# Kernel optimization log

Measured on AMD Instinct MI355X. Metric: run time of the kernel, lower is better.

## Reference

```python
import jax, jax.numpy as jnp
import numpy as np

K = 3  # Chebyshev filter size (max_view)


def avwgcn(X, E, weights_pool, bias_pool):
    """Adaptive node-wise graph conv. X: [B,N,C_in], E: [N,D]."""
    N = E.shape[0]
    # adaptive adjacency: softmax over rows of relu(E E^T)
    supports = jax.nn.softmax(jax.nn.relu(E @ E.T), axis=1)  # [N,N]
    support_set = [jnp.eye(N, dtype=X.dtype), supports]
    for _ in range(2, K):  # Chebyshev recursion
        support_set.append(2.0 * supports @ support_set[-1] - support_set[-2])
    S = jnp.stack(support_set, axis=0)  # [K,N,N]
    W = jnp.einsum('nd,dkio->nkio', E, weights_pool)  # per-node weights [N,K,Ci,Co]
    bias = E @ bias_pool  # [N,Co]
    XG = jnp.einsum('knm,bmc->bnkc', S, X)  # [B,N,K,Ci]
    return jnp.einsum('bnki,nkio->bno', XG, W) + bias  # [B,N,Co]


def setup_inputs() -> dict:
    key = jax.random.key(0)
    ks = jax.random.split(key, 5)
    B, N, Cin, Cout, D = 32, 4096, 2, 64, 10
    Ci = Cin + Cout  # 66
    X = jax.random.normal(ks[0], (B, N, Cin), dtype=jnp.float32)
    H = jnp.zeros((B, N, Cout), dtype=jnp.float32)
    E = jax.random.normal(ks[1], (N, D), dtype=jnp.float32)
    W_gate = jax.random.normal(ks[2], (D, K, Ci, 2 * Cout), dtype=jnp.float32) * 0.1
    b_gate = jnp.zeros((D, 2 * Cout), dtype=jnp.float32)
    W_update = jax.random.normal(ks[3], (D, K, Ci, Cout), dtype=jnp.float32) * 0.1
    b_update = jnp.zeros((D, Cout), dtype=jnp.float32)
    return {"X": X, "H": H, "E": E, "W_gate": W_gate, "b_gate": b_gate,
            "W_update": W_update, "b_update": b_update}


def reference(X, H, E, W_gate, b_gate, W_update, b_update):
    Cout = H.shape[-1]
    XH = jnp.concatenate([X, H], axis=-1)  # [B,N,Cin+Cout]
    ZR = jax.nn.sigmoid(avwgcn(XH, E, W_gate, b_gate))  # [B,N,2*Cout]
    Z, R = ZR[..., :Cout], ZR[..., Cout:]
    C = jnp.concatenate([X, Z * H], axis=-1)
    HC = jnp.tanh(avwgcn(C, E, W_update, b_update))
    return R * H + (1.0 - R) * HC
```

## Files before the change

### kernel.cpp

```cpp
#include <hip/hip_runtime.h>
#include <math.h>

#define N_NODES 4096
#define BATCH   32
#define D_EMB   10
#define CIN     2
#define COUT    64
#define CI      66
#define KSUP    3
#define NCOLS   2112
#define NPAD    2176
#define LDT     4096

#define KI_REAL 198
#define KILD    232
#define OCH     (32 * KILD)
#define WROW_G  (128 * KILD)
#define WROW_U  (64 * KILD)
#define WGT2_R  (WROW_G + WROW_U)

typedef _Float16 half_t;
typedef __attribute__((ext_vector_type(8))) _Float16 f16x8;
typedef __attribute__((ext_vector_type(4))) _Float16 f16x4;
typedef __attribute__((ext_vector_type(2))) _Float16 f16x2;
typedef __attribute__((ext_vector_type(4))) float f32x4;

union u32h2 { unsigned u; f16x2 h; };

__device__ __forceinline__ float fast_sigmoid(float x) { return 1.f / (1.f + __expf(-x)); }
__device__ __forceinline__ float fast_tanh(float x) { return 1.f - 2.f / (__expf(2.f * x) + 1.f); }

__device__ __forceinline__ void gld_lds16(const half_t* g, half_t* l) {
  __builtin_amdgcn_global_load_lds(
      (const __attribute__((address_space(1))) void*)g,
      (__attribute__((address_space(3))) void*)l, 16, 0, 0);
}

__global__ __launch_bounds__(256) void k_softmax_p(const float* __restrict__ E,
                                                   half_t* __restrict__ Pb) {
  const int n = blockIdx.x;
  const int tid = threadIdx.x;
  __shared__ float En[D_EMB];
  __shared__ float ms[256], ss[256];
  if (tid < D_EMB) En[tid] = E[n * D_EMB + tid];
  __syncthreads();
  float en[D_EMB];
#pragma unroll
  for (int d = 0; d < D_EMB; ++d) en[d] = En[d];

  float m = -1e30f, s = 0.f;
  for (int c = tid; c < N_NODES; c += 256) {
    const float* Ec = E + c * D_EMB;
    float v = 0.f;
#pragma unroll
    for (int d = 0; d < D_EMB; ++d) v += en[d] * Ec[d];
    v = fmaxf(v, 0.f);
    if (v > m) { s *= __expf(m - v); m = v; }
    s += __expf(v - m);
  }
  ms[tid] = m; ss[tid] = s;
  __syncthreads();
  for (int off = 128; off > 0; off >>= 1) {
    if (tid < off) {
      float m2 = ms[tid + off], s2 = ss[tid + off];
      float m1 = ms[tid], s1 = ss[tid];
      float mm = fmaxf(m1, m2);
      ms[tid] = mm;
      ss[tid] = s1 * __expf(m1 - mm) + s2 * __expf(m2 - mm);
    }
    __syncthreads();
  }
  const float M = ms[0];
  const float inv = 1.f / ss[0];
  half_t* Pr = Pb + (size_t)n * N_NODES;
  for (int c = tid; c < N_NODES; c += 256) {
    const float* Ec = E + c * D_EMB;
    float v = 0.f;
#pragma unroll
    for (int d = 0; d < D_EMB; ++d) v += en[d] * Ec[d];
    v = fmaxf(v, 0.f);
    Pr[c] = (half_t)(__expf(v - M) * inv);
  }
}

__global__ __launch_bounds__(256) void k_build_v0(const float* __restrict__ X,
                                                  const float* __restrict__ H,
                                                  half_t* __restrict__ Vt,
                                                  half_t* __restrict__ Vn,
                                                  half_t* __restrict__ Cbt,
                                                  half_t* __restrict__ Cbn) {
  size_t idx = (size_t)blockIdx.x * 256 + threadIdx.x;
  if (idx >= (size_t)N_NODES * NCOLS) return;
  const int m = (int)(idx / NCOLS);
  const int col = (int)(idx % NCOLS);
  const int b = col / CI;
  const int c = col % CI;
  float v;
  if (c < CIN) v = X[((size_t)b * N_NODES + m) * CIN + c];
  else         v = H[((size_t)b * N_NODES + m) * COUT + (c - CIN)];
  const half_t h = (half_t)v;
  Vn[(size_t)m * NPAD + col] = h;
  Vt[(size_t)col * LDT + m] = h;
  if (c < CIN) {
    Cbn[(size_t)m * NPAD + col] = h;
    Cbt[(size_t)col * LDT + m] = h;
  }
}

__global__ __launch_bounds__(256) void k_gemm_f16(const half_t* __restrict__ A,
                                                  const half_t* __restrict__ Bt,
                                                  half_t* __restrict__ Cn,
                                                  half_t* __restrict__ Ct) {
  __shared__ half_t As[128 * 32];
  __shared__ half_t Bs[128 * 32];
  const int tid = threadIdx.x;
  const int lane = tid & 63;
  const int wave = tid >> 6;
  const int wm = (wave >> 1) * 64;
  const int wn = (wave & 1) * 64;
  const int rb = blockIdx.y * 128;
  const int cb = blockIdx.x * 128;

  const int srow = lane >> 2;
  const int skg = (((lane & 3) + ((lane >> 3) & 3)) & 3) * 8;
  const half_t* ga0 = A + (size_t)(rb + wave * 32 + srow) * N_NODES + skg;
  const half_t* ga1 = ga0 + (size_t)16 * N_NODES;
  const half_t* gb0 = Bt + (size_t)(cb + wave * 32 + srow) * LDT + skg;
  const half_t* gb1 = gb0 + (size_t)16 * LDT;
  half_t* lA0 = As + wave * 1024;
  half_t* lA1 = lA0 + 512;
  half_t* lB0 = Bs + wave * 1024;
  half_t* lB1 = lB0 + 512;

  const int fr = lane & 15;
  const int fg = lane >> 4;
  const int fofs = (4 * fr + ((fg - (fr >> 1)) & 3)) * 8;

  f32x4 acc[4][4] = {};

  for (int k0 = 0; k0 < N_NODES; k0 += 32) {
    __syncthreads();
    gld_lds16(ga0 + k0, lA0);
    gld_lds16(ga1 + k0, lA1);
    gld_lds16(gb0 + k0, lB0);
    gld_lds16(gb1 + k0, lB1);
    __syncthreads();

    f16x8 a[4], b[4];
#pragma unroll
    for (int i = 0; i < 4; ++i)
      a[i] = *(const f16x8*)&As[((wm >> 4) + i) * 512 + fofs];
#pragma unroll
    for (int j = 0; j < 4; ++j)
      b[j] = *(const f16x8*)&Bs[((wn >> 4) + j) * 512 + fofs];
#pragma unroll
    for (int i = 0; i < 4; ++i)
#pragma unroll
      for (int j = 0; j < 4; ++j)
        acc[i][j] = __builtin_amdgcn_mfma_f32_16x16x32_f16(a[i], b[j], acc[i][j], 0, 0, 0);
  }

  const int en = lane & 15;
  const int em = (lane >> 4) * 4;
#pragma unroll
  for (int i = 0; i < 4; ++i) {
#pragma unroll
    for (int j = 0; j < 4; ++j) {
      const int m0 = rb + wm + i * 16 + em;
      const int n = cb + wn + j * 16 + en;
      half_t h0 = (half_t)acc[i][j][0];
      half_t h1 = (half_t)acc[i][j][1];
      half_t h2 = (half_t)acc[i][j][2];
      half_t h3 = (half_t)acc[i][j][3];
      if (Ct) {
        f16x4 t4 = {h0, h1, h2, h3};
        *(f16x4*)&Ct[(size_t)n * LDT + m0] = t4;
      }
      Cn[(size_t)(m0 + 0) * NPAD + n] = h0;
      Cn[(size_t)(m0 + 1) * NPAD + n] = h1;
      Cn[(size_t)(m0 + 2) * NPAD + n] = h2;
      Cn[(size_t)(m0 + 3) * NPAD + n] = h3;
    }
  }
}

__global__ __launch_bounds__(256) void k_wgt2(const float* __restrict__ Wg,
                                              const float* __restrict__ Wu,
                                              unsigned* __restrict__ WT2) {
  const int r = blockIdx.x * 256 + threadIdx.x;
  if (r >= WGT2_R) return;
  const float* pool;
  int o, ki, ostr;
  if (r < WROW_G) { o = r / KILD; ki = r % KILD; pool = Wg; ostr = 128; }
  else { int r2 = r - WROW_G; o = r2 / KILD; ki = r2 % KILD; pool = Wu; ostr = 64; }
#pragma unroll
  for (int dp = 0; dp < 5; ++dp) {
    u32h2 v; v.h = f16x2{(half_t)0.f, (half_t)0.f};
    if (ki < KI_REAL) {
      const int k = ki / CI;
      const int i = ki % CI;
      v.h[0] = (half_t)pool[(((size_t)(2 * dp) * KSUP + k) * CI + i) * ostr + o];
      v.h[1] = (half_t)pool[(((size_t)(2 * dp + 1) * KSUP + k) * CI + i) * ostr + o];
    }
    WT2[(size_t)dp * WGT2_R + r] = v.u;
  }
}

__device__ __forceinline__ void stage_xg(const half_t* __restrict__ v0r,
                                         const half_t* __restrict__ g1r,
                                         const half_t* __restrict__ g2r,
                                         half_t* __restrict__ xg, int tid) {
  for (int idx = tid; idx < NCOLS / 8; idx += 256) {
    const f16x8 v0 = *(const f16x8*)&v0r[idx * 8];
    const f16x8 g1 = *(const f16x8*)&g1r[idx * 8];
    const f16x8 g2 = *(const f16x8*)&g2r[idx * 8];
    const f16x8 x2 = g2 + g2 - v0;
#pragma unroll
    for (int e = 0; e < 8; ++e) {
      const int col = idx * 8 + e;
      const int b = col / CI;
      const int i = col - b * CI;
      xg[b * KILD + i] = v0[e];
      xg[b * KILD + CI + i] = g1[e];
      xg[b * KILD + 2 * CI + i] = x2[e];
    }
  }
  for (int z = tid; z < 32 * 17; z += 256) {
    const int b = z / 17;
    const int j = z - b * 17;
    *(unsigned*)&xg[b * KILD + KI_REAL + j * 2] = 0u;
  }
}

__global__ __launch_bounds__(256) void k_gate_t(const half_t* __restrict__ Vn,
                                                const half_t* __restrict__ G1n,
                                                const half_t* __restrict__ G2n,
                                                const unsigned* __restrict__ WT2,
                                                const float* __restrict__ E,
                                                const float* __restrict__ bg,
                                                const float* __restrict__ H,
                                                half_t* __restrict__ Cbn,
                                                half_t* __restrict__ Cbt,
                                                half_t* __restrict__ Rb) {
  const int n0 = blockIdx.x * 2;
  const int tid = threadIdx.x;
  const int lane = tid & 63;
  const int wave = tid >> 6;
  __shared__ half_t Wl[2][OCH];
  __shared__ half_t xg[2][OCH];
  __shared__ float biasl[2][128];

  f16x2 e2p0[5], e2p1[5];
#pragma unroll
  for (int dp = 0; dp < 5; ++dp) {
    e2p0[dp][0] = (half_t)E[n0 * D_EMB + 2 * dp];
    e2p0[dp][1] = (half_t)E[n0 * D_EMB + 2 * dp + 1];
    e2p1[dp][0] = (half_t)E[(n0 + 1) * D_EMB + 2 * dp];
    e2p1[dp][1] = (half_t)E[(n0 + 1) * D_EMB + 2 * dp + 1];
  }

  {
    const int nn = tid >> 7;
    const int o = tid & 127;
    float s = 0.f;
#pragma unroll
    for (int d = 0; d < D_EMB; ++d) s += E[(n0 + nn) * D_EMB + d] * bg[d * 128 + o];
    biasl[nn][o] = s;
  }
  stage_xg(Vn + (size_t)n0 * NPAD, G1n + (size_t)n0 * NPAD, G2n + (size_t)n0 * NPAD, xg[0], tid);
  stage_xg(Vn + (size_t)(n0 + 1) * NPAD, G1n + (size_t)(n0 + 1) * NPAD, G2n + (size_t)(n0 + 1) * NPAD, xg[1], tid);

  const int fr = lane & 15;
  const int fk = (lane >> 4) * 8;
  const int en = lane & 15;
  const int em = (lane >> 4) * 4;
  const int node = wave & 1;
  const int ot = wave >> 1;
  const int nn = n0 + node;

#pragma unroll
  for (int p = 0; p < 4; ++p) {
    if (p > 0) __syncthreads();
    for (int base = tid * 8; base < OCH; base += 2048) {
      float a0[8] = {}, a1[8] = {};
#pragma unroll
      for (int dp = 0; dp < 5; ++dp) {
        const unsigned* wrow = WT2 + (size_t)dp * WGT2_R + p * OCH + base;
        uint4 wa = *(const uint4*)wrow;
        uint4 wb = *(const uint4*)(wrow + 4);
        u32h2 c0, c1, c2, c3;
        c0.u = wa.x; c1.u = wa.y; c2.u = wa.z; c3.u = wa.w;
        a0[0] = __builtin_amdgcn_fdot2(c0.h, e2p0[dp], a0[0], false);
        a0[1] = __builtin_amdgcn_fdot2(c1.h, e2p0[dp], a0[1], false);
        a0[2] = __builtin_amdgcn_fdot2(c2.h, e2p0[dp], a0[2], false);
        a0[3] = __builtin_amdgcn_fdot2(c3.h, e2p0[dp], a0[3], false);
        a1[0] = __builtin_amdgcn_fdot2(c0.h, e2p1[dp], a1[0], false);
        a1[1] = __builtin_amdgcn_fdot2(c1.h, e2p1[dp], a1[1], false);
        a1[2] = __builtin_amdgcn_fdot2(c2.h, e2p1[dp], a1[2], false);
        a1[3] = __builtin_amdgcn_fdot2(c3.h, e2p1[dp], a1[3], false);
        c0.u = wb.x; c1.u = wb.y; c2.u = wb.z; c3.u = wb.w;
        a0[4] = __builtin_amdgcn_fdot2(c0.h, e2p0[dp], a0[4], false);
        a0[5] = __builtin_amdgcn_fdot2(c1.h, e2p0[dp], a0[5], false);
        a0[6] = __builtin_amdgcn_fdot2(c2.h, e2p0[dp], a0[6], false);
        a0[7] = __builtin_amdgcn_fdot2(c3.h, e2p0[dp], a0[7], false);
        a1[4] = __builtin_amdgcn_fdot2(c0.h, e2p1[dp], a1[4], false);
        a1[5] = __builtin_amdgcn_fdot2(c1.h, e2p1[dp], a1[5], false);
        a1[6] = __builtin_amdgcn_fdot2(c2.h, e2p1[dp], a1[6], false);
        a1[7] = __builtin_amdgcn_fdot2(c3.h, e2p1[dp], a1[7], false);
      }
      f16x8 w0, w1;
#pragma unroll
      for (int e = 0; e < 8; ++e) { w0[e] = (half_t)a0[e]; w1[e] = (half_t)a1[e]; }
      *(f16x8*)&Wl[0][base] = w0;
      *(f16x8*)&Wl[1][base] = w1;
    }
    __syncthreads();

    f32x4 acc2[2] = {};
#pragma unroll
    for (int ks = 0; ks < 7; ++ks) {
      const f16x8 a0 = *(const f16x8*)&xg[node][fr * KILD + ks * 32 + fk];
      const f16x8 a1 = *(const f16x8*)&xg[node][(16 + fr) * KILD + ks * 32 + fk];
      const f16x8 b0 = *(const f16x8*)&Wl[node][(ot * 16 + fr) * KILD + ks * 32 + fk];
      acc2[0] = __builtin_amdgcn_mfma_f32_16x16x32_f16(a0, b0, acc2[0], 0, 0, 0);
      acc2[1] = __builtin_amdgcn_mfma_f32_16x16x32_f16(a1, b0, acc2[1], 0, 0, 0);
    }
    const int o_g = p * 32 + ot * 16 + en;
    const float bo = biasl[node][o_g];
#pragma unroll
    for (int i = 0; i < 2; ++i)
#pragma unroll
      for (int r = 0; r < 4; ++r) {
        const int b = i * 16 + em + r;
        const float s = fast_sigmoid(acc2[i][r] + bo);
        if (p < 2) {
          const float hv = H[((size_t)b * N_NODES + nn) * COUT + o_g];
          const half_t z = (half_t)(s * hv);
          const int c0 = b * CI + CIN + o_g;
          Cbn[(size_t)nn * NPAD + c0] = z;
          Cbt[(size_t)c0 * LDT + nn] = z;
        } else {
          Rb[((size_t)b * N_NODES + nn) * COUT + (o_g - 64)] = (half_t)s;
        }
      }
  }
}

__global__ __launch_bounds__(256) void k_update_t(const half_t* __restrict__ Cbn,
                                                  const half_t* __restrict__ G1n,
                                                  const half_t* __restrict__ G2n,
                                                  const unsigned* __restrict__ WT2,
                                                  const float* __restrict__ E,
                                                  const float* __restrict__ bu,
                                                  const float* __restrict__ H,
                                                  const half_t* __restrict__ Rb,
                                                  float* __restrict__ Out) {
  const int n0 = blockIdx.x * 2;
  const int tid = threadIdx.x;
  const int lane = tid & 63;
  const int wave = tid >> 6;
  __shared__ half_t Wl[2][OCH];
  __shared__ half_t xg[2][OCH];
  __shared__ float biasl[2][64];

  f16x2 e2p0[5], e2p1[5];
#pragma unroll
  for (int dp = 0; dp < 5; ++dp) {
    e2p0[dp][0] = (half_t)E[n0 * D_EMB + 2 * dp];
    e2p0[dp][1] = (half_t)E[n0 * D_EMB + 2 * dp + 1];
    e2p1[dp][0] = (half_t)E[(n0 + 1) * D_EMB + 2 * dp];
    e2p1[dp][1] = (half_t)E[(n0 + 1) * D_EMB + 2 * dp + 1];
  }

  if (tid < 128) {
    const int nn = tid >> 6;
    const int o = tid & 63;
    float s = 0.f;
#pragma unroll
    for (int d = 0; d < D_EMB; ++d) s += E[(n0 + nn) * D_EMB + d] * bu[d * COUT + o];
    biasl[nn][o] = s;
  }
  stage_xg(Cbn + (size_t)n0 * NPAD, G1n + (size_t)n0 * NPAD, G2n + (size_t)n0 * NPAD, xg[0], tid);
  stage_xg(Cbn + (size_t)(n0 + 1) * NPAD, G1n + (size_t)(n0 + 1) * NPAD, G2n + (size_t)(n0 + 1) * NPAD, xg[1], tid);

  const int fr = lane & 15;
  const int fk = (lane >> 4) * 8;
  const int en = lane & 15;
  const int em = (lane >> 4) * 4;
  const int node = wave & 1;
  const int ot = wave >> 1;
  const int nn = n0 + node;

#pragma unroll
  for (int p = 0; p < 2; ++p) {
    if (p > 0) __syncthreads();
    for (int base = tid * 8; base < OCH; base += 2048) {
      float a0[8] = {}, a1[8] = {};
#pragma unroll
      for (int dp = 0; dp < 5; ++dp) {
        const unsigned* wrow = WT2 + (size_t)dp * WGT2_R + WROW_G + p * OCH + base;
        uint4 wa = *(const uint4*)wrow;
        uint4 wb = *(const uint4*)(wrow + 4);
        u32h2 c0, c1, c2, c3;
        c0.u = wa.x; c1.u = wa.y; c2.u = wa.z; c3.u = wa.w;
        a0[0] = __builtin_amdgcn_fdot2(c0.h, e2p0[dp], a0[0], false);
        a0[1] = __builtin_amdgcn_fdot2(c1.h, e2p0[dp], a0[1], false);
        a0[2] = __builtin_amdgcn_fdot2(c2.h, e2p0[dp], a0[2], false);
        a0[3] = __builtin_amdgcn_fdot2(c3.h, e2p0[dp], a0[3], false);
        a1[0] = __builtin_amdgcn_fdot2(c0.h, e2p1[dp], a1[0], false);
        a1[1] = __builtin_amdgcn_fdot2(c1.h, e2p1[dp], a1[1], false);
        a1[2] = __builtin_amdgcn_fdot2(c2.h, e2p1[dp], a1[2], false);
        a1[3] = __builtin_amdgcn_fdot2(c3.h, e2p1[dp], a1[3], false);
        c0.u = wb.x; c1.u = wb.y; c2.u = wb.z; c3.u = wb.w;
        a0[4] = __builtin_amdgcn_fdot2(c0.h, e2p0[dp], a0[4], false);
        a0[5] = __builtin_amdgcn_fdot2(c1.h, e2p0[dp], a0[5], false);
        a0[6] = __builtin_amdgcn_fdot2(c2.h, e2p0[dp], a0[6], false);
        a0[7] = __builtin_amdgcn_fdot2(c3.h, e2p0[dp], a0[7], false);
        a1[4] = __builtin_amdgcn_fdot2(c0.h, e2p1[dp], a1[4], false);
        a1[5] = __builtin_amdgcn_fdot2(c1.h, e2p1[dp], a1[5], false);
        a1[6] = __builtin_amdgcn_fdot2(c2.h, e2p1[dp], a1[6], false);
        a1[7] = __builtin_amdgcn_fdot2(c3.h, e2p1[dp], a1[7], false);
      }
      f16x8 w0, w1;
#pragma unroll
      for (int e = 0; e < 8; ++e) { w0[e] = (half_t)a0[e]; w1[e] = (half_t)a1[e]; }
      *(f16x8*)&Wl[0][base] = w0;
      *(f16x8*)&Wl[1][base] = w1;
    }
    __syncthreads();

    f32x4 acc2[2] = {};
#pragma unroll
    for (int ks = 0; ks < 7; ++ks) {
      const f16x8 a0 = *(const f16x8*)&xg[node][fr * KILD + ks * 32 + fk];
      const f16x8 a1 = *(const f16x8*)&xg[node][(16 + fr) * KILD + ks * 32 + fk];
      const f16x8 b0 = *(const f16x8*)&Wl[node][(ot * 16 + fr) * KILD + ks * 32 + fk];
      acc2[0] = __builtin_amdgcn_mfma_f32_16x16x32_f16(a0, b0, acc2[0], 0, 0, 0);
      acc2[1] = __builtin_amdgcn_mfma_f32_16x16x32_f16(a1, b0, acc2[1], 0, 0, 0);
    }
    const int o = p * 32 + ot * 16 + en;
    const float bo = biasl[node][o];
#pragma unroll
    for (int i = 0; i < 2; ++i)
#pragma unroll
      for (int r = 0; r < 4; ++r) {
        const int b = i * 16 + em + r;
        const float hc = fast_tanh(acc2[i][r] + bo);
        const size_t base = ((size_t)b * N_NODES + nn) * COUT + o;
        const float hv = H[base];
        const float rr = (float)Rb[base];
        Out[base] = rr * hv + (1.f - rr) * hc;
      }
  }
}

extern "C" void kernel_launch(void* const* d_in, const int* in_sizes, int n_in,
                              void* d_out, int out_size, void* d_ws, size_t ws_size,
                              hipStream_t stream) {
  const float* X  = (const float*)d_in[0];
  const float* H  = (const float*)d_in[1];
  const float* E  = (const float*)d_in[2];
  const float* Wg = (const float*)d_in[3];
  const float* bg = (const float*)d_in[4];
  const float* Wu = (const float*)d_in[5];
  const float* bu = (const float*)d_in[6];
  float* out = (float*)d_out;

  const size_t SZ_P = (size_t)N_NODES * N_NODES;
  const size_t SZ_M = (size_t)NPAD * LDT;
  half_t* Pb  = (half_t*)d_ws;
  half_t* Vt  = Pb + SZ_P;
  half_t* Vn  = Vt + SZ_M;
  half_t* G1t = Vn + SZ_M;
  half_t* G1n = G1t + SZ_M;
  half_t* G2n = G1n + SZ_M;
  half_t* Cbt = G2n + SZ_M;
  half_t* Cbn = Cbt + SZ_M;
  half_t* Rb  = Cbn + SZ_M;
  unsigned* WT2 = (unsigned*)(Rb + (size_t)BATCH * N_NODES * COUT);

  k_softmax_p<<<N_NODES, 256, 0, stream>>>(E, Pb);
  {
    const size_t tot = (size_t)N_NODES * NCOLS;
    k_build_v0<<<(int)((tot + 255) / 256), 256, 0, stream>>>(X, H, Vt, Vn, Cbt, Cbn);
  }
  k_wgt2<<<(WGT2_R + 255) / 256, 256, 0, stream>>>(Wg, Wu, WT2);

  dim3 gg(NPAD / 128, N_NODES / 128);
  k_gemm_f16<<<gg, 256, 0, stream>>>(Pb, Vt, G1n, G1t);
  k_gemm_f16<<<gg, 256, 0, stream>>>(Pb, G1t, G2n, nullptr);
  k_gate_t<<<N_NODES / 2, 256, 0, stream>>>(Vn, G1n, G2n, WT2, E, bg, H, Cbn, Cbt, Rb);
  k_gemm_f16<<<gg, 256, 0, stream>>>(Pb, Cbt, G1n, G1t);
  k_gemm_f16<<<gg, 256, 0, stream>>>(Pb, G1t, G2n, nullptr);
  k_update_t<<<N_NODES / 2, 256, 0, stream>>>(Cbn, G1n, G2n, WT2, E, bu, H, Rb, out);
}
```

Measured before the change: 827.3 us.

## Triple-buffer LDS in fp16 GEMM with async prefetch and block swizzle

Replaces the two-barrier-per-step GEMM loop with a three-stage LDS ring buffer, where global-to-LDS loads run two k-tiles ahead and a single vmcnt wait plus barrier guards each step. It also remaps the block index with an XCD-aware swizzle so neighbouring tiles share L2, and raises wave priority around the MFMA burst. The aim is to hide global load latency behind matrix math, at the cost of three times the LDS footprint and a hardcoded tile count and grid shape.

```diff
diff --git a/kernel.cpp b/kernel.cpp
--- a/kernel.cpp
+++ b/kernel.cpp
@@ -107,19 +107,45 @@
   }
 }
 
+__device__ __forceinline__ void gemm_compute_tile(const half_t* __restrict__ Lb,
+                                                  int wm, int wn, int fofs,
+                                                  f32x4 (&acc)[4][4]) {
+  const half_t* As_ = Lb;
+  const half_t* Bs_ = Lb + 4096;
+  f16x8 a[4], b[4];
+#pragma unroll
+  for (int i = 0; i < 4; ++i)
+    a[i] = *(const f16x8*)&As_[((wm >> 4) + i) * 512 + fofs];
+#pragma unroll
+  for (int j = 0; j < 4; ++j)
+    b[j] = *(const f16x8*)&Bs_[((wn >> 4) + j) * 512 + fofs];
+  __builtin_amdgcn_s_setprio(1);
+#pragma unroll
+  for (int i = 0; i < 4; ++i)
+#pragma unroll
+    for (int j = 0; j < 4; ++j)
+      acc[i][j] = __builtin_amdgcn_mfma_f32_16x16x32_f16(a[i], b[j], acc[i][j], 0, 0, 0);
+  __builtin_amdgcn_s_setprio(0);
+}
+
 __global__ __launch_bounds__(256) void k_gemm_f16(const half_t* __restrict__ A,
                                                   const half_t* __restrict__ Bt,
                                                   half_t* __restrict__ Cn,
                                                   half_t* __restrict__ Ct) {
-  __shared__ half_t As[128 * 32];
-  __shared__ half_t Bs[128 * 32];
+  __shared__ half_t LB[3][8192];
   const int tid = threadIdx.x;
   const int lane = tid & 63;
   const int wave = tid >> 6;
+
+  int flat = blockIdx.y * 17 + blockIdx.x;
+  flat = (flat & 7) * 68 + (flat >> 3);
+  const int bx = flat % 17;
+  const int by = flat / 17;
+
   const int wm = (wave >> 1) * 64;
   const int wn = (wave & 1) * 64;
-  const int rb = blockIdx.y * 128;
-  const int cb = blockIdx.x * 128;
+  const int rb = by * 128;
+  const int cb = bx * 128;
 
   const int srow = lane >> 2;
   const int skg = (((lane & 3) + ((lane >> 3) & 3)) & 3) * 8;
@@ -127,10 +153,10 @@
   const half_t* ga1 = ga0 + (size_t)16 * N_NODES;
   const half_t* gb0 = Bt + (size_t)(cb + wave * 32 + srow) * LDT + skg;
   const half_t* gb1 = gb0 + (size_t)16 * LDT;
-  half_t* lA0 = As + wave * 1024;
-  half_t* lA1 = lA0 + 512;
-  half_t* lB0 = Bs + wave * 1024;
-  half_t* lB1 = lB0 + 512;
+  const int lA0 = wave * 1024;
+  const int lA1 = lA0 + 512;
+  const int lB0 = 4096 + wave * 1024;
+  const int lB1 = lB0 + 512;
 
   const int fr = lane & 15;
   const int fg = lane >> 4;
@@ -138,27 +164,31 @@
 
   f32x4 acc[4][4] = {};
 
-  for (int k0 = 0; k0 < N_NODES; k0 += 32) {
-    __syncthreads();
-    gld_lds16(ga0 + k0, lA0);
-    gld_lds16(ga1 + k0, lA1);
-    gld_lds16(gb0 + k0, lB0);
-    gld_lds16(gb1 + k0, lB1);
-    __syncthreads();
-
-    f16x8 a[4], b[4];
-#pragma unroll
-    for (int i = 0; i < 4; ++i)
-      a[i] = *(const f16x8*)&As[((wm >> 4) + i) * 512 + fofs];
-#pragma unroll
-    for (int j = 0; j < 4; ++j)
-      b[j] = *(const f16x8*)&Bs[((wn >> 4) + j) * 512 + fofs];
-#pragma unroll
-    for (int i = 0; i < 4; ++i)
-#pragma unroll
-      for (int j = 0; j < 4; ++j)
-        acc[i][j] = __builtin_amdgcn_mfma_f32_16x16x32_f16(a[i], b[j], acc[i][j], 0, 0, 0);
-  }
+#define STAGE_T(buf, kk) do { half_t* Lp = LB[(buf)]; \
+    gld_lds16(ga0 + (kk), Lp + lA0); gld_lds16(ga1 + (kk), Lp + lA1); \
+    gld_lds16(gb0 + (kk), Lp + lB0); gld_lds16(gb1 + (kk), Lp + lB1); } while (0)
+
+  STAGE_T(0, 0);
+  STAGE_T(1, 32);
+
+  for (int t = 0; t < 126; t += 3) {
+    asm volatile("s_waitcnt vmcnt(4)\n\ts_barrier" ::: "memory");
+    STAGE_T(2, (t + 2) * 32);
+    gemm_compute_tile(LB[0], wm, wn, fofs, acc);
+
+    asm volatile("s_waitcnt vmcnt(4)\n\ts_barrier" ::: "memory");
+    STAGE_T(0, (t + 3) * 32);
+    gemm_compute_tile(LB[1], wm, wn, fofs, acc);
+
+    asm volatile("s_waitcnt vmcnt(4)\n\ts_barrier" ::: "memory");
+    STAGE_T(1, (t + 4) * 32);
+    gemm_compute_tile(LB[2], wm, wn, fofs, acc);
+  }
+  asm volatile("s_waitcnt vmcnt(4)\n\ts_barrier" ::: "memory");
+  gemm_compute_tile(LB[0], wm, wn, fofs, acc);
+  asm volatile("s_waitcnt vmcnt(0)\n\ts_barrier" ::: "memory");
+  gemm_compute_tile(LB[1], wm, wn, fofs, acc);
+#undef STAGE_T
 
   const int en = lane & 15;
   const int em = (lane >> 4) * 4;
```

After: 802.8 us. 1.03x faster.
